# Kernel tuning notes

Measured on AMD Instinct MI355X. Metric: run time of the kernel, lower is better.

Reference implementation:

```python
import jax, jax.numpy as jnp
import numpy as np

SIGMA = 0.1
B = 1.0
SPATIAL_WEIGHT = 0.5
EPS = 1e-5


def setup_inputs() -> dict:
    key = jax.random.key(0)
    k1, k2 = jax.random.split(key)
    N, C, H, W = 2, 256, 64, 64
    I_features = jax.random.normal(k1, (N, C, H, W), dtype=jnp.float32)
    T_features = jax.random.normal(k2, (N, C, H, W), dtype=jnp.float32)
    return {"I_features": I_features, "T_features": T_features}


def _calc_cx(raw):
    # raw: [N, P_T, H, W]; min + exp-softmax over the target-patch axis (axis=1)
    mn = jnp.min(raw, axis=1, keepdims=True)
    rel = raw / (mn + EPS)
    w = jnp.exp((B - rel) / SIGMA)
    return w / jnp.sum(w, axis=1, keepdims=True)


def reference(I_features, T_features):
    N, C, H, W = I_features.shape
    P = H * W

    # ---- spatial branch: L2 distances on a normalized meshgrid (C=2) ----
    rows = jnp.arange(H, dtype=jnp.float32) / (H + 1)
    cols = jnp.arange(W, dtype=jnp.float32) / (W + 1)
    grid = jnp.stack(jnp.meshgrid(rows, cols, indexing="ij"))  # [2, H, W]
    g = grid.reshape(2, P)                                      # [2, P]
    sq = jnp.sum(g * g, axis=0)                                 # [P]
    d = sq[:, None] + sq[None, :] - 2.0 * (g.T @ g)             # [P_I, P_T]
    d = jnp.clip(d, 0.0)
    raw_sp = d.T.reshape(1, P, H, W)  # [1, P_T, H, W]; identical per sample
    cx_sp = _calc_cx(raw_sp)

    # ---- feature branch: cosine similarity via centered, L2-normed feats ----
    meanT = jnp.mean(T_features, axis=(0, 2, 3), keepdims=True)
    Ic = I_features - meanT
    Tc = T_features - meanT
    In = Ic / jnp.linalg.norm(Ic, axis=1, keepdims=True)
    Tn = Tc / jnp.linalg.norm(Tc, axis=1, keepdims=True)
    Iv = In.reshape(N, C, P)
    Tv = Tn.reshape(N, C, P)
    dot = jnp.einsum("ncq,ncp->nqp", Tv, Iv)  # [N, P_T, P_I]
    raw_feat = ((1.0 - dot) / 2.0).reshape(N, P, H, W)
    cx_feat = _calc_cx(raw_feat)

    # ---- combine, max over I positions, mean over T patches, -log, mean ----
    cx = (1.0 - SPATIAL_WEIGHT) * cx_feat + SPATIAL_WEIGHT * cx_sp  # [N,P,H,W]
    m = jnp.max(cx, axis=(2, 3))  # [N, P]
    m = jnp.mean(m, axis=1)       # [N]
    return jnp.mean(-jnp.log(m))
```

## Files before the change

kernel.cpp:

```cpp
#include <hip/hip_runtime.h>
#include <math.h>

#define PP 4096
#define CC 256
#define NN 2
#define NSTEP 16

typedef __attribute__((ext_vector_type(4))) float f32x4;
typedef __attribute__((ext_vector_type(8))) int i32x8;

__device__ __forceinline__ void gld_lds16(const char* g, char* l) {
    __builtin_amdgcn_global_load_lds(
        (const __attribute__((address_space(1))) unsigned int*)g,
        (__attribute__((address_space(3))) unsigned int*)l, 16, 0, 0);
}


__global__ __launch_bounds__(256) void mean_kernel(const float* __restrict__ T,
                                                   float* __restrict__ meanT,
                                                   float* __restrict__ loss_acc) {
    int c = blockIdx.x, tid = threadIdx.x;
    float s = 0.f;
    for (int n = 0; n < NN; n++) {
        const float4* Tc = (const float4*)&T[(size_t)(n * CC + c) * PP];
        for (int g = 0; g < 4; g++) {
            float4 v = Tc[tid + g * 256];
            s += (v.x + v.y) + (v.z + v.w);
        }
    }
    __shared__ float red[256];
    red[tid] = s; __syncthreads();
    for (int st = 128; st > 0; st >>= 1) {
        if (tid < st) red[tid] += red[tid + st];
        __syncthreads();
    }
    if (tid == 0) meanT[c] = red[0] * (1.0f / (NN * PP));
    if (blockIdx.x == 0 && tid < NN) loss_acc[tid] = 0.f;
}

__global__ __launch_bounds__(256) void normalize_kernel(const float* __restrict__ I,
                                                        const float* __restrict__ T,
                                                        const float* __restrict__ meanT,
                                                        char* __restrict__ InT,
                                                        char* __restrict__ TnT) {
    int pc = blockIdx.x * 32;
    int n = blockIdx.y;
    int which = blockIdx.z;
    const float* X = which ? T : I;
    char* Y = which ? TnT : InT;

    __shared__ float tile[CC][36];
    __shared__ float red[32][32];
    __shared__ float invn[32];

    int tid = threadIdx.x;
    int pl4 = tid & 7, c0 = tid >> 3;
    float sq0 = 0.f, sq1 = 0.f, sq2 = 0.f, sq3 = 0.f;
    for (int c = c0; c < CC; c += 32) {
        float m = meanT[c];
        float4 v = *(const float4*)&X[(size_t)(n * CC + c) * PP + pc + pl4 * 4];
        v.x -= m; v.y -= m; v.z -= m; v.w -= m;
        *(float4*)&tile[c][pl4 * 4] = v;
        sq0 += v.x * v.x; sq1 += v.y * v.y; sq2 += v.z * v.z; sq3 += v.w * v.w;
    }
    red[c0][pl4 * 4 + 0] = sq0;
    red[c0][pl4 * 4 + 1] = sq1;
    red[c0][pl4 * 4 + 2] = sq2;
    red[c0][pl4 * 4 + 3] = sq3;
    __syncthreads();
    if (tid < 32) {
        float s = 0.f;
        for (int k = 0; k < 32; k++) s += red[k][tid];
        invn[tid] = 1.0f / sqrtf(s);
    }
    __syncthreads();
    for (int pass = 0; pass < 8; pass++) {
        int r = pass * 4 + (tid >> 6);
        int c4 = (tid & 63) * 4;
        float in = invn[r];
        float v0 = tile[c4 + 0][r] * in;
        float v1 = tile[c4 + 1][r] * in;
        float v2 = tile[c4 + 2][r] * in;
        float v3 = tile[c4 + 3][r] * in;
        int w = __builtin_amdgcn_cvt_pk_fp8_f32(v0, v1, 0, false);
        w = __builtin_amdgcn_cvt_pk_fp8_f32(v2, v3, w, true);
        *(unsigned*)&Y[(size_t)(n * PP + pc + r) * CC + c4] = (unsigned)w;
    }
}

__global__ __launch_bounds__(512) void cx_strip(const char* __restrict__ TnT,
                                                const char* __restrict__ InT,
                                                float* __restrict__ loss_acc) {
    const int strip = blockIdx.x;
    const int n = blockIdx.y;
    const int p0 = strip * 32;
    const char* __restrict__ Ab = TnT + (size_t)n * PP * CC;
    const char* __restrict__ Bb = InT + (size_t)n * PP * CC + (size_t)p0 * CC;

    __shared__ __align__(16) char Aw[8][2][8192];
    __shared__ __align__(16) char Bsm[8192];
    __shared__ float redw[8][32];
    __shared__ float inv2s[32];
    __shared__ float dwl[32];

    const int tid = threadIdx.x;
    const int l = tid & 63, wv = tid >> 6;
    const int lm = l & 15, quad = l >> 4;
    const int lr4 = l >> 4;
    const int sl = l & 15;

    const char* asrc[8];
#pragma unroll
    for (int g = 0; g < 8; g++) {
        int row = g * 4 + lr4;
        asrc[g] = Ab + (size_t)(wv * 32 + row) * 256 + ((sl ^ (row & 15)) * 16);
    }
#define STAGE_A(qs, b)                                                        \
    {                                                                         \
        char* dbase_ = &Aw[wv][b][0];                                         \
        _Pragma("unroll")                                                     \
        for (int g_ = 0; g_ < 8; g_++)                                        \
            gld_lds16(asrc[g_] + (size_t)(qs) * 65536, dbase_ + g_ * 1024);   \
    }

    int aoff[16];
#pragma unroll
    for (int i = 0; i < 2; i++)
#pragma unroll
        for (int kb = 0; kb < 2; kb++)
#pragma unroll
            for (int j = 0; j < 4; j++)
                aoff[i * 8 + kb * 4 + j] =
                    (i * 16 + lm) * 256 +
                    (((kb * 8 + j * 2 + (quad >> 1)) ^ lm) * 16) + (quad & 1) * 8;

    {
        int rB = wv * 4 + lr4;
        gld_lds16(Bb + rB * 256 + ((sl ^ (rB & 15)) * 16), &Bsm[wv * 1024]);
    }
    STAGE_A(0, 0);
    __syncthreads();

    union BU { long l[2][8]; i32x8 v[2][2]; } bfu;
#pragma unroll
    for (int ct = 0; ct < 2; ct++)
#pragma unroll
        for (int ks = 0; ks < 8; ks++) {
            int g8 = ks * 4 + quad;
            int row = ct * 16 + lm;
            bfu.l[ct][ks] = *(const long*)&Bsm[row * 256 +
                             (((g8 >> 1) ^ (row & 15)) * 16) + (g8 & 1) * 8];
        }

    float amax[2] = {-3.4e38f, -3.4e38f};
    float hc[2] = {0.f, 0.f}, c0c[2] = {0.f, 0.f};
    float ss[2] = {0.f, 0.f};
    const int qd = p0 >> 8;
    const int wd = (p0 >> 5) & 7;

#pragma unroll 1
    for (int pass = 0; pass < 2; pass++) {
        if (pass == 1) STAGE_A(0, 0);
#pragma unroll 1
        for (int qs = 0; qs < NSTEP; qs++) {
            if (qs < NSTEP - 1) {
                STAGE_A(qs + 1, (qs + 1) & 1);
                asm volatile("s_waitcnt vmcnt(8)" ::: "memory");
            } else {
                asm volatile("s_waitcnt vmcnt(0)" ::: "memory");
            }
            __builtin_amdgcn_sched_barrier(0);

            const char* Ac = &Aw[wv][qs & 1][0];
            f32x4 acc[2][2] = {};
#pragma unroll
            for (int kb = 0; kb < 2; kb++) {
                union AU { long l[4]; i32x8 v; } a_[2];
#pragma unroll
                for (int j = 0; j < 4; j++)
#pragma unroll
                    for (int i = 0; i < 2; i++)
                        a_[i].l[j] = *(const long*)&Ac[aoff[i * 8 + kb * 4 + j]];
#pragma unroll
                for (int i = 0; i < 2; i++)
#pragma unroll
                    for (int ct = 0; ct < 2; ct++)
                        acc[i][ct] = __builtin_amdgcn_mfma_scale_f32_16x16x128_f8f6f4(
                            a_[i].v, bfu.v[ct][kb], acc[i][ct],
                            0, 0,
                            0, 0x7f7f7f7f,
                            0, 0x7f7f7f7f);
            }
            if (pass == 0) {
#pragma unroll
                for (int ct = 0; ct < 2; ct++)
#pragma unroll
                    for (int i = 0; i < 2; i++)
#pragma unroll
                        for (int e = 0; e < 4; e++)
                            amax[ct] = fmaxf(amax[ct], acc[i][ct][e]);
            } else {
#pragma unroll
                for (int ct = 0; ct < 2; ct++) {
                    float s2 = 0.f;
#pragma unroll
                    for (int i = 0; i < 2; i++)
#pragma unroll
                        for (int e = 0; e < 4; e++)
                            s2 += exp2f(fmaf(acc[i][ct][e], hc[ct], c0c[ct]));
                    ss[ct] += s2;
                }
                if ((qs == qd) && (wv == wd)) {
#pragma unroll
                    for (int ct = 0; ct < 2; ct++)
                        if (quad == (lm >> 2))
                            dwl[ct * 16 + lm] = exp2f(
                                fmaf(acc[ct][ct][lm & 3], hc[ct], c0c[ct]));
                }
            }
        }

        if (pass == 0) {
#pragma unroll
            for (int ct = 0; ct < 2; ct++) {
                amax[ct] = fmaxf(amax[ct], __shfl_xor(amax[ct], 16));
                amax[ct] = fmaxf(amax[ct], __shfl_xor(amax[ct], 32));
                if (quad == 0) redw[wv][ct * 16 + lm] = amax[ct];
            }
            __syncthreads();
            if (tid < 32) {
                float mx = redw[0][tid];
#pragma unroll
                for (int w2 = 1; w2 < 8; w2++) mx = fmaxf(mx, redw[w2][tid]);
                float mnv = (1.0f - mx) * 0.5f;
                inv2s[tid] = 14.4269504f / (mnv + 1e-5f);
            }
            __syncthreads();
            {
                float i20 = inv2s[lm], i21 = inv2s[16 + lm];
                hc[0] = i20 * 0.5f; c0c[0] = 14.4269504f - hc[0];
                hc[1] = i21 * 0.5f; c0c[1] = 14.4269504f - hc[1];
            }
        }
    }

#pragma unroll
    for (int ct = 0; ct < 2; ct++) {
        ss[ct] += __shfl_xor(ss[ct], 16);
        ss[ct] += __shfl_xor(ss[ct], 32);
        if (quad == 0) redw[wv][ct * 16 + lm] = ss[ct];
    }
    __syncthreads();
    if (tid < 32) {
        float s = 0.f;
#pragma unroll
        for (int w2 = 0; w2 < 8; w2++) s += redw[w2][tid];
        float part = dwl[tid] / s;
        part += __shfl_xor(part, 1);
        part += __shfl_xor(part, 2);
        part += __shfl_xor(part, 4);
        part += __shfl_xor(part, 8);
        part += __shfl_xor(part, 16);
        if (tid == 0) atomicAdd(&loss_acc[n], part);
    }
#undef STAGE_A
}

__global__ void finalize_kernel(const float* __restrict__ loss_acc,
                                float* __restrict__ out) {
    float m0 = 0.5f + 0.5f * (loss_acc[0] / (float)PP);
    float m1 = 0.5f + 0.5f * (loss_acc[1] / (float)PP);
    out[0] = 0.5f * (-logf(m0) - logf(m1));
}

extern "C" void kernel_launch(void* const* d_in, const int* in_sizes, int n_in,
                              void* d_out, int out_size, void* d_ws, size_t ws_size,
                              hipStream_t stream) {
    const float* I = (const float*)d_in[0];
    const float* T = (const float*)d_in[1];
    float* out = (float*)d_out;

    char* ws = (char*)d_ws;
    const size_t SZ_F8 = (size_t)NN * PP * CC;
    char* InT = ws;
    char* TnT = ws + SZ_F8;
    float* meanT = (float*)(ws + 2 * SZ_F8);
    float* loss_acc = (float*)(ws + 2 * SZ_F8 + 32768);

    mean_kernel<<<CC, 256, 0, stream>>>(T, meanT, loss_acc);
    normalize_kernel<<<dim3(PP / 32, NN, 2), 256, 0, stream>>>(I, T, meanT, InT, TnT);
    cx_strip<<<dim3(PP / 32, NN), 512, 0, stream>>>(TnT, InT, loss_acc);
    finalize_kernel<<<1, 1, 0, stream>>>(loss_acc, out);
}
```

Before: 108.2 us.

## Split cx_strip work across 16 waves with 16-row A tiles per wave

Doubles the cx_strip block to 1024 threads (16 waves). Each wave now stages and multiplies 16 target rows per step instead of 32, which halves the per-wave MFMA, exp and LDS-load work and the per-wave staging buffer. The diagonal-term capture is reindexed for the new wave mapping and the reductions now span 16 waves. The goal is more latency hiding and in-flight loads per CU. In exchange it adds more cross-wave reduction and barrier cost, and fewer independent MFMAs per wave to overlap with loads.

```diff
diff --git a/kernel.cpp b/kernel.cpp
--- a/kernel.cpp
+++ b/kernel.cpp
@@ -88,18 +88,18 @@
     }
 }
 
-__global__ __launch_bounds__(512) void cx_strip(const char* __restrict__ TnT,
-                                                const char* __restrict__ InT,
-                                                float* __restrict__ loss_acc) {
+__global__ __launch_bounds__(1024) void cx_strip(const char* __restrict__ TnT,
+                                                 const char* __restrict__ InT,
+                                                 float* __restrict__ loss_acc) {
     const int strip = blockIdx.x;
     const int n = blockIdx.y;
     const int p0 = strip * 32;
     const char* __restrict__ Ab = TnT + (size_t)n * PP * CC;
     const char* __restrict__ Bb = InT + (size_t)n * PP * CC + (size_t)p0 * CC;
 
-    __shared__ __align__(16) char Aw[8][2][8192];
+    __shared__ __align__(16) char Aw[16][2][4096];
     __shared__ __align__(16) char Bsm[8192];
-    __shared__ float redw[8][32];
+    __shared__ float redw[16][32];
     __shared__ float inv2s[32];
     __shared__ float dwl[32];
 
@@ -109,32 +109,29 @@
     const int lr4 = l >> 4;
     const int sl = l & 15;
 
-    const char* asrc[8];
-#pragma unroll
-    for (int g = 0; g < 8; g++) {
+    const char* asrc[4];
+#pragma unroll
+    for (int g = 0; g < 4; g++) {
         int row = g * 4 + lr4;
-        asrc[g] = Ab + (size_t)(wv * 32 + row) * 256 + ((sl ^ (row & 15)) * 16);
+        asrc[g] = Ab + (size_t)(wv * 16 + row) * 256 + ((sl ^ (row & 15)) * 16);
     }
 #define STAGE_A(qs, b)                                                        \
     {                                                                         \
         char* dbase_ = &Aw[wv][b][0];                                         \
         _Pragma("unroll")                                                     \
-        for (int g_ = 0; g_ < 8; g_++)                                        \
+        for (int g_ = 0; g_ < 4; g_++)                                        \
             gld_lds16(asrc[g_] + (size_t)(qs) * 65536, dbase_ + g_ * 1024);   \
     }
 
-    int aoff[16];
-#pragma unroll
-    for (int i = 0; i < 2; i++)
-#pragma unroll
-        for (int kb = 0; kb < 2; kb++)
-#pragma unroll
-            for (int j = 0; j < 4; j++)
-                aoff[i * 8 + kb * 4 + j] =
-                    (i * 16 + lm) * 256 +
-                    (((kb * 8 + j * 2 + (quad >> 1)) ^ lm) * 16) + (quad & 1) * 8;
-
-    {
+    int aoff[8];
+#pragma unroll
+    for (int kb = 0; kb < 2; kb++)
+#pragma unroll
+        for (int j = 0; j < 4; j++)
+            aoff[kb * 4 + j] = lm * 256 +
+                (((kb * 8 + j * 2 + (quad >> 1)) ^ lm) * 16) + (quad & 1) * 8;
+
+    if (wv < 8) {
         int rB = wv * 4 + lr4;
         gld_lds16(Bb + rB * 256 + ((sl ^ (rB & 15)) * 16), &Bsm[wv * 1024]);
     }
@@ -155,8 +152,8 @@
     float amax[2] = {-3.4e38f, -3.4e38f};
     float hc[2] = {0.f, 0.f}, c0c[2] = {0.f, 0.f};
     float ss[2] = {0.f, 0.f};
-    const int qd = p0 >> 8;
-    const int wd = (p0 >> 5) & 7;
+    const int qdd0 = p0 >> 8, wdd0 = (p0 >> 4) & 15;
+    const int qdd1 = (p0 + 16) >> 8, wdd1 = ((p0 + 16) >> 4) & 15;
 
 #pragma unroll 1
     for (int pass = 0; pass < 2; pass++) {
@@ -165,58 +162,47 @@
         for (int qs = 0; qs < NSTEP; qs++) {
             if (qs < NSTEP - 1) {
                 STAGE_A(qs + 1, (qs + 1) & 1);
-                asm volatile("s_waitcnt vmcnt(8)" ::: "memory");
+                asm volatile("s_waitcnt vmcnt(4)" ::: "memory");
             } else {
                 asm volatile("s_waitcnt vmcnt(0)" ::: "memory");
             }
             __builtin_amdgcn_sched_barrier(0);
 
             const char* Ac = &Aw[wv][qs & 1][0];
-            f32x4 acc[2][2] = {};
+            f32x4 acc[2] = {};
 #pragma unroll
             for (int kb = 0; kb < 2; kb++) {
-                union AU { long l[4]; i32x8 v; } a_[2];
+                union AU { long l[4]; i32x8 v; } a_;
 #pragma unroll
                 for (int j = 0; j < 4; j++)
-#pragma unroll
-                    for (int i = 0; i < 2; i++)
-                        a_[i].l[j] = *(const long*)&Ac[aoff[i * 8 + kb * 4 + j]];
-#pragma unroll
-                for (int i = 0; i < 2; i++)
-#pragma unroll
-                    for (int ct = 0; ct < 2; ct++)
-                        acc[i][ct] = __builtin_amdgcn_mfma_scale_f32_16x16x128_f8f6f4(
-                            a_[i].v, bfu.v[ct][kb], acc[i][ct],
-                            0, 0,
-                            0, 0x7f7f7f7f,
-                            0, 0x7f7f7f7f);
+                    a_.l[j] = *(const long*)&Ac[aoff[kb * 4 + j]];
+#pragma unroll
+                for (int ct = 0; ct < 2; ct++)
+                    acc[ct] = __builtin_amdgcn_mfma_scale_f32_16x16x128_f8f6f4(
+                        a_.v, bfu.v[ct][kb], acc[ct],
+                        0, 0,
+                        0, 0x7f7f7f7f,
+                        0, 0x7f7f7f7f);
             }
             if (pass == 0) {
 #pragma unroll
                 for (int ct = 0; ct < 2; ct++)
 #pragma unroll
-                    for (int i = 0; i < 2; i++)
-#pragma unroll
-                        for (int e = 0; e < 4; e++)
-                            amax[ct] = fmaxf(amax[ct], acc[i][ct][e]);
+                    for (int e = 0; e < 4; e++)
+                        amax[ct] = fmaxf(amax[ct], acc[ct][e]);
             } else {
 #pragma unroll
                 for (int ct = 0; ct < 2; ct++) {
                     float s2 = 0.f;
 #pragma unroll
-                    for (int i = 0; i < 2; i++)
-#pragma unroll
-                        for (int e = 0; e < 4; e++)
-                            s2 += exp2f(fmaf(acc[i][ct][e], hc[ct], c0c[ct]));
+                    for (int e = 0; e < 4; e++)
+                        s2 += exp2f(fmaf(acc[ct][e], hc[ct], c0c[ct]));
                     ss[ct] += s2;
                 }
-                if ((qs == qd) && (wv == wd)) {
-#pragma unroll
-                    for (int ct = 0; ct < 2; ct++)
-                        if (quad == (lm >> 2))
-                            dwl[ct * 16 + lm] = exp2f(
-                                fmaf(acc[ct][ct][lm & 3], hc[ct], c0c[ct]));
-                }
+                if (qs == qdd0 && wv == wdd0 && quad == (lm >> 2))
+                    dwl[lm] = exp2f(fmaf(acc[0][lm & 3], hc[0], c0c[0]));
+                if (qs == qdd1 && wv == wdd1 && quad == (lm >> 2))
+                    dwl[16 + lm] = exp2f(fmaf(acc[1][lm & 3], hc[1], c0c[1]));
             }
         }
 
@@ -231,7 +217,7 @@
             if (tid < 32) {
                 float mx = redw[0][tid];
 #pragma unroll
-                for (int w2 = 1; w2 < 8; w2++) mx = fmaxf(mx, redw[w2][tid]);
+                for (int w2 = 1; w2 < 16; w2++) mx = fmaxf(mx, redw[w2][tid]);
                 float mnv = (1.0f - mx) * 0.5f;
                 inv2s[tid] = 14.4269504f / (mnv + 1e-5f);
             }
@@ -254,7 +240,7 @@
     if (tid < 32) {
         float s = 0.f;
 #pragma unroll
-        for (int w2 = 0; w2 < 8; w2++) s += redw[w2][tid];
+        for (int w2 = 0; w2 < 16; w2++) s += redw[w2][tid];
         float part = dwl[tid] / s;
         part += __shfl_xor(part, 1);
         part += __shfl_xor(part, 2);
@@ -289,6 +275,6 @@
 
     mean_kernel<<<CC, 256, 0, stream>>>(T, meanT, loss_acc);
     normalize_kernel<<<dim3(PP / 32, NN, 2), 256, 0, stream>>>(I, T, meanT, InT, TnT);
-    cx_strip<<<dim3(PP / 32, NN), 512, 0, stream>>>(TnT, InT, loss_acc);
+    cx_strip<<<dim3(PP / 32, NN), 1024, 0, stream>>>(TnT, InT, loss_acc);
     finalize_kernel<<<1, 1, 0, stream>>>(loss_acc, out);
 }
```

Result: faster. 105.4 us (-2.6%).
